# Optimization experiments

Measured on AMD Instinct MI355X. Metric: run time of the kernel, lower is better.

The kernel has to match this reference:

```python
import jax, jax.numpy as jnp
import numpy as np

N_NODES = 8192
IN_F = 256
OUT_F = 256
ALPHA = 0.2  # LeakyReLU negative slope


def setup_inputs() -> dict:
    key = jax.random.key(0)
    k1, k2, k3, k4 = jax.random.split(key, 4)
    X = jax.random.normal(k1, (N_NODES, IN_F), dtype=jnp.float32)
    A = jax.random.randint(k2, (N_NODES, N_NODES), 0, 2, dtype=jnp.int32)
    # torch nn.Linear weight layout: (out_features, in_features)
    W = jax.random.normal(k3, (OUT_F, IN_F), dtype=jnp.float32) * (1.0 / np.sqrt(IN_F))
    r = jax.random.normal(k4, (2 * OUT_F, 1), dtype=jnp.float32)
    return {"X": X, "A": A, "W": W, "r": r}


def reference(X, A, W, r):
    # Wh = X @ W^T  -> (N, F_out)
    Wh = X @ W.T
    # Split r so that cat([Wh_i, Wh_j]) @ r == Wh_i @ r_src + Wh_j @ r_dst
    F_out = Wh.shape[-1]
    r_src = r[:F_out, 0]   # (F,)
    r_dst = r[F_out:, 0]   # (F,)
    s_i = Wh @ r_src       # (N,)
    s_j = Wh @ r_dst       # (N,)
    e = s_i[:, None] + s_j[None, :]                      # (N, N)
    e = jnp.where(e >= 0, e, ALPHA * e)                  # LeakyReLU
    e = jnp.where(A == 0, -jnp.inf, e)                   # mask non-edges
    attention = jax.nn.softmax(e, axis=1)                # row-wise softmax
    output = attention @ Wh                              # (N, F_out)
    return jax.nn.gelu(output, approximate=False)        # torch F.gelu (exact)
```

## Files before the change

### kernel.cpp

```cpp
#include <hip/hip_runtime.h>
#include <hip/hip_bf16.h>

#define N_NODES 8192
#define NF      256
#define L2E     1.44269504088896341f

typedef __attribute__((ext_vector_type(8))) short short8;
typedef __attribute__((ext_vector_type(4))) short short4v;
typedef __attribute__((ext_vector_type(4))) float floatx4;

static __device__ __forceinline__ float bf2f(short s) {
    return __uint_as_float(((unsigned)(unsigned short)s) << 16);
}
static __device__ __forceinline__ short f2bf_rn(float f) {
    unsigned u = __float_as_uint(f) + 0x8000u;
    return (short)(u >> 16);
}
struct bfpair { short hi, lo; };
static __device__ __forceinline__ bfpair split_bf(float x) {
    bfpair p;
    p.hi = f2bf_rn(x);
    p.lo = f2bf_rn(x - bf2f(p.hi));
    return p;
}
static __device__ __forceinline__ void async16(const void* g, void* l) {
    __builtin_amdgcn_global_load_lds(
        (const __attribute__((address_space(1))) unsigned*)g,
        (__attribute__((address_space(3))) unsigned*)l, 16, 0, 0);
}

__global__ __launch_bounds__(256) void kx_split(const float* __restrict__ W,
                                                short* __restrict__ Whi,
                                                short* __restrict__ Wlo) {
    #pragma unroll
    for (int e = 0; e < 4; ++e) {
        const int i = blockIdx.x * 1024 + e * 256 + threadIdx.x;
        bfpair p = split_bf(W[i]);
        Whi[i] = p.hi;
        Wlo[i] = p.lo;
    }
}

__global__ __launch_bounds__(512) void k1_gemm(const float* __restrict__ X,
                                               const short* __restrict__ Whi,
                                               const short* __restrict__ Wlo,
                                               const float* __restrict__ r,
                                               short* __restrict__ WhT,
                                               float* __restrict__ sp_src,
                                               float* __restrict__ sp_dst) {
    __shared__ float Xs[32 * 256];

    const int tid = threadIdx.x;
    const int w = tid >> 6, lane = tid & 63;
    const int q = lane >> 4, m = lane & 15;
    const int rh = w >> 2, cq = w & 3;
    const int i_base = blockIdx.x * 32;

    #pragma unroll
    for (int v = 0; v < 4; ++v) {
        const int rowv = w * 4 + v;
        const int c = lane ^ (rowv & 7);
        async16(X + (size_t)(i_base + rowv) * NF + c * 4, &Xs[rowv * 256]);
    }
    __syncthreads();

    floatx4 acc[4] = {};
    const int xrow = rh * 16 + m;
    const int r7 = xrow & 7;
    #pragma unroll
    for (int ks = 0; ks < 8; ++ks) {
        const int c0 = ks * 8 + q * 2;
        float4 f0 = *(const float4*)(&Xs[xrow * 256 + ((c0 ^ r7) * 4)]);
        float4 f1 = *(const float4*)(&Xs[xrow * 256 + (((c0 + 1) ^ r7) * 4)]);
        const float xsv[8] = {f0.x, f0.y, f0.z, f0.w, f1.x, f1.y, f1.z, f1.w};
        short8 xh, xl;
        #pragma unroll
        for (int c = 0; c < 8; ++c) {
            bfpair p = split_bf(xsv[c]);
            xh[c] = p.hi; xl[c] = p.lo;
        }
        #pragma unroll
        for (int nt = 0; nt < 4; ++nt) {
            const int n = cq * 64 + nt * 16 + m;
            short8 wh = *(const short8*)(Whi + n * NF + ks * 32 + q * 8);
            short8 wl = *(const short8*)(Wlo + n * NF + ks * 32 + q * 8);
            acc[nt] = __builtin_amdgcn_mfma_f32_16x16x32_bf16(xh, wh, acc[nt], 0, 0, 0);
            acc[nt] = __builtin_amdgcn_mfma_f32_16x16x32_bf16(xl, wh, acc[nt], 0, 0, 0);
            acc[nt] = __builtin_amdgcn_mfma_f32_16x16x32_bf16(xh, wl, acc[nt], 0, 0, 0);
        }
    }

    const int i0 = i_base + rh * 16 + q * 4;
    float vs[4] = {0.f, 0.f, 0.f, 0.f}, vd[4] = {0.f, 0.f, 0.f, 0.f};
    #pragma unroll
    for (int nt = 0; nt < 4; ++nt) {
        const int n = cq * 64 + nt * 16 + m;
        short4v v;
        #pragma unroll
        for (int r2 = 0; r2 < 4; ++r2) v[r2] = f2bf_rn(acc[nt][r2]);
        *(short4v*)(WhT + (size_t)n * N_NODES + i0) = v;
        const float rs = r[n], rd = r[NF + n];
        #pragma unroll
        for (int r2 = 0; r2 < 4; ++r2) {
            vs[r2] = fmaf(acc[nt][r2], rs, vs[r2]);
            vd[r2] = fmaf(acc[nt][r2], rd, vd[r2]);
        }
    }
    #pragma unroll
    for (int mask = 1; mask <= 8; mask <<= 1) {
        #pragma unroll
        for (int r2 = 0; r2 < 4; ++r2) {
            vs[r2] += __shfl_xor(vs[r2], mask);
            vd[r2] += __shfl_xor(vd[r2], mask);
        }
    }
    if (m == 0) {
        #pragma unroll
        for (int r2 = 0; r2 < 4; ++r2) {
            sp_src[cq * N_NODES + i0 + r2] = vs[r2];
            sp_dst[cq * N_NODES + i0 + r2] = vd[r2];
        }
    }
}

__global__ __launch_bounds__(256) void k2_sv(const float* __restrict__ sp_src,
                                             const float* __restrict__ sp_dst,
                                             float* __restrict__ s_src,
                                             float* __restrict__ s_dst,
                                             float* __restrict__ pmax) {
    __shared__ float red[256];
    const int tid = threadIdx.x;
    const int i = blockIdx.x * 256 + tid;
    float ss = 0.f, sd = 0.f;
    #pragma unroll
    for (int nb = 0; nb < 4; ++nb) {
        ss += sp_src[nb * N_NODES + i];
        sd += sp_dst[nb * N_NODES + i];
    }
    s_src[i] = ss;
    s_dst[i] = sd;
    red[tid] = sd;
    __syncthreads();
    for (int off = 128; off > 0; off >>= 1) {
        if (tid < off) red[tid] = fmaxf(red[tid], red[tid + off]);
        __syncthreads();
    }
    if (tid == 0) pmax[blockIdx.x] = red[0];
}

static __device__ __forceinline__ void pgroup(const int4 a, const floatx4 t,
                                              const float s_i, const float d_i,
                                              float* p) {
    const int av[4] = {a.x, a.y, a.z, a.w};
    #pragma unroll
    for (int c = 0; c < 4; ++c) {
        float sum = s_i + t[c];
        float lr  = fmaxf(sum, 0.2f * sum);
        float pp  = __builtin_amdgcn_exp2f(fmaf(lr, L2E, d_i));
        p[c] = (av[c] != 0) ? pp : 0.0f;
    }
}

__global__ __launch_bounds__(512, 4) void k4_attn(const int* __restrict__ Adj,
                                                  const short* __restrict__ WhT,
                                                  const float* __restrict__ s_dst,
                                                  const float* __restrict__ s_src,
                                                  const float* __restrict__ pmax,
                                                  float* __restrict__ pden,
                                                  float* __restrict__ outacc) {
    __shared__ short Bs[2][256][64];

    const int tid = threadIdx.x;
    const int w = tid >> 6, lane = tid & 63;
    const int q = lane >> 4, m = lane & 15;
    const int rh = w >> 1, ch = w & 1;
    const int ib = blockIdx.x & 127;
    const int jh = blockIdx.x >> 7;
    const int i0 = ib * 64;
    const int jbase = jh * 2048;
    const int row = i0 + rh * 16 + m;

    float M = pmax[0];
    #pragma unroll
    for (int b = 1; b < 32; ++b) M = fmaxf(M, pmax[b]);
    const float s_i = s_src[row];
    const float e0 = s_i + M;
    const float d_i = -fmaxf(e0, 0.2f * e0) * L2E;

    const int srow = lane >> 3;
    const int scc = (lane & 7) ^ srow;
    const short* gB[4];
    #pragma unroll
    for (int v = 0; v < 4; ++v)
        gB[v] = WhT + (size_t)(w * 32 + v * 8 + srow) * N_NODES + jbase + scc * 8;

    const int* Ap = Adj + (size_t)row * N_NODES + jbase + q * 8;
    const float* tp = s_dst + jbase + q * 8;

    floatx4 acc[8];
    #pragma unroll
    for (int nt = 0; nt < 8; ++nt) acc[nt] = (floatx4){0.f, 0.f, 0.f, 0.f};
    float den = 0.f;

    #pragma unroll
    for (int v = 0; v < 4; ++v)
        async16(gB[v], &Bs[0][w * 32 + v * 8][0]);
    int4 a0 = *(const int4*)(Ap);
    int4 a1 = *(const int4*)(Ap + 4);
    int4 a2 = *(const int4*)(Ap + 32);
    int4 a3 = *(const int4*)(Ap + 36);
    __syncthreads();

    for (int s = 0; s < 32; ++s) {
        const int cur = s & 1;
        const int gt = s * 64;

        floatx4 t0 = *(const floatx4*)(tp + gt);
        floatx4 t1 = *(const floatx4*)(tp + gt + 4);
        floatx4 t2 = *(const floatx4*)(tp + gt + 32);
        floatx4 t3 = *(const floatx4*)(tp + gt + 36);
        __builtin_amdgcn_sched_barrier(0);

        short* dstb = &Bs[cur ^ 1][0][0];
        const int gn = ((s + 1) & 31) * 64;
        #pragma unroll
        for (int v = 0; v < 4; ++v)
            async16(gB[v] + gn, dstb + (w * 32 + v * 8) * 64);
        __builtin_amdgcn_sched_barrier(0);

        int4 na0 = *(const int4*)(Ap + gn);
        int4 na1 = *(const int4*)(Ap + gn + 4);
        int4 na2 = *(const int4*)(Ap + gn + 32);
        int4 na3 = *(const int4*)(Ap + gn + 36);
        __builtin_amdgcn_sched_barrier(0);

        float p[16];
        pgroup(a0, t0, s_i, d_i, p);
        pgroup(a1, t1, s_i, d_i, p + 4);
        pgroup(a2, t2, s_i, d_i, p + 8);
        pgroup(a3, t3, s_i, d_i, p + 12);

        short8 af0, af1;
        #pragma unroll
        for (int c = 0; c < 8; ++c) { af0[c] = f2bf_rn(p[c]); af1[c] = f2bf_rn(p[8 + c]); }
        #pragma unroll
        for (int c = 0; c < 16; ++c) den += p[c];

        const short* Bb = &Bs[cur][0][0];
        __builtin_amdgcn_s_setprio(1);
        #pragma unroll
        for (int nt = 0; nt < 8; ++nt) {
            const int n = ch * 128 + nt * 16 + m;
            const int sw = m & 7;
            short8 b0 = *(const short8*)(Bb + n * 64 + ((q ^ sw) * 8));
            short8 b1 = *(const short8*)(Bb + n * 64 + (((4 + q) ^ sw) * 8));
            acc[nt] = __builtin_amdgcn_mfma_f32_16x16x32_bf16(af0, b0, acc[nt], 0, 0, 0);
            acc[nt] = __builtin_amdgcn_mfma_f32_16x16x32_bf16(af1, b1, acc[nt], 0, 0, 0);
        }
        __builtin_amdgcn_s_setprio(0);

        __builtin_amdgcn_sched_barrier(0);
        asm volatile("s_waitcnt vmcnt(4)" ::: "memory");
        __builtin_amdgcn_s_barrier();

        a0 = na0; a1 = na1; a2 = na2; a3 = na3;
    }

    den += __shfl_xor(den, 16);
    den += __shfl_xor(den, 32);
    if (ch == 0 && q == 0) pden[jh * N_NODES + row] = den;

    #pragma unroll
    for (int nt = 0; nt < 8; ++nt) {
        #pragma unroll
        for (int rg = 0; rg < 4; ++rg) {
            const int orow = i0 + rh * 16 + q * 4 + rg;
            const int n = ch * 128 + nt * 16 + m;
            atomicAdd(&outacc[(size_t)orow * NF + n], acc[nt][rg]);
        }
    }
}

__global__ __launch_bounds__(256) void k5_fin(const float* __restrict__ pden,
                                              float* __restrict__ out) {
    const int gid = blockIdx.x * 256 + threadIdx.x;
    const int row = gid >> 5;
    const int c0 = (gid & 31) * 8;
    const float d = (pden[row] + pden[N_NODES + row]) +
                    (pden[2 * N_NODES + row] + pden[3 * N_NODES + row]);
    const float inv = 1.0f / fmaxf(d, 1e-30f);
    float* p = out + (size_t)row * NF + c0;
    float4 v0 = *(const float4*)(p);
    float4 v1 = *(const float4*)(p + 4);
    float xs[8] = {v0.x, v0.y, v0.z, v0.w, v1.x, v1.y, v1.z, v1.w};
    #pragma unroll
    for (int c = 0; c < 8; ++c) {
        const float x = xs[c] * inv;
        xs[c] = 0.5f * x * (1.0f + erff(x * 0.70710678118f));
    }
    *(float4*)(p)     = (float4){xs[0], xs[1], xs[2], xs[3]};
    *(float4*)(p + 4) = (float4){xs[4], xs[5], xs[6], xs[7]};
}

extern "C" void kernel_launch(void* const* d_in, const int* in_sizes, int n_in,
                              void* d_out, int out_size, void* d_ws, size_t ws_size,
                              hipStream_t stream) {
    const float* X = (const float*)d_in[0];
    const int*   A = (const int*)d_in[1];
    const float* W = (const float*)d_in[2];
    const float* r = (const float*)d_in[3];
    float* out = (float*)d_out;

    char* wsp = (char*)d_ws;
    short* WhT    = (short*)wsp;                    wsp += (size_t)NF * N_NODES * 2;
    short* Whi    = (short*)wsp;                    wsp += NF * NF * 2;
    short* Wlo    = (short*)wsp;                    wsp += NF * NF * 2;
    float* sp_src = (float*)wsp;                    wsp += 4 * N_NODES * 4;
    float* sp_dst = (float*)wsp;                    wsp += 4 * N_NODES * 4;
    float* s_src  = (float*)wsp;                    wsp += N_NODES * 4;
    float* s_dst  = (float*)wsp;                    wsp += N_NODES * 4;
    float* pmax   = (float*)wsp;
    float* pden   = sp_src;

    hipMemsetAsync(out, 0, (size_t)N_NODES * NF * 4, stream);
    kx_split<<<64, 256, 0, stream>>>(W, Whi, Wlo);
    k1_gemm<<<256, 512, 0, stream>>>(X, Whi, Wlo, r, WhT, sp_src, sp_dst);
    k2_sv<<<32, 256, 0, stream>>>(sp_src, sp_dst, s_src, s_dst, pmax);
    k4_attn<<<512, 512, 0, stream>>>(A, WhT, s_dst, s_src, pmax, pden, out);
    k5_fin<<<1024, 256, 0, stream>>>(pden, out);
}
```

Measured before the change: 476.9 us.

## Pack adjacency into bitmask in a pre-pass and stage s_dst in LDS

Adds a k3_bits kernel that uses wave ballots to compress the int32 adjacency matrix into a per-row bitmask. The attention kernel then reads 2 mask words per step instead of 16 int32 values. It also stages the block's s_dst slice into shared memory once, instead of loading it from global memory every iteration. The full 256MB adjacency read still happens, now in a separate streaming kernel, so the intent is to take the large mask traffic out of the MFMA loop, at the cost of an extra launch and an 8MB intermediate write and read.

```diff
diff --git a/kernel.cpp b/kernel.cpp
--- a/kernel.cpp
+++ b/kernel.cpp
@@ -148,20 +148,33 @@
     if (tid == 0) pmax[blockIdx.x] = red[0];
 }
 
-static __device__ __forceinline__ void pgroup(const int4 a, const floatx4 t,
-                                              const float s_i, const float d_i,
-                                              float* p) {
-    const int av[4] = {a.x, a.y, a.z, a.w};
+__global__ __launch_bounds__(512) void k3_bits(const int* __restrict__ Adj,
+                                               unsigned* __restrict__ mask) {
+    const int w = threadIdx.x >> 6, lane = threadIdx.x & 63;
+    const int row = blockIdx.x * 8 + w;
+    const int* Ar = Adj + (size_t)row * N_NODES;
+    unsigned long long* Mr = (unsigned long long*)(mask + (size_t)row * 256);
+    for (int it = 0; it < 128; ++it) {
+        const int v = Ar[it * 64 + lane];
+        const unsigned long long b = __ballot(v != 0);
+        if (lane == 0) Mr[it] = b;
+    }
+}
+
+static __device__ __forceinline__ void pgroupb(const unsigned bits, const int sh,
+                                               const floatx4 t,
+                                               const float s_i, const float d_i,
+                                               float* p) {
     #pragma unroll
     for (int c = 0; c < 4; ++c) {
         float sum = s_i + t[c];
         float lr  = fmaxf(sum, 0.2f * sum);
         float pp  = __builtin_amdgcn_exp2f(fmaf(lr, L2E, d_i));
-        p[c] = (av[c] != 0) ? pp : 0.0f;
-    }
-}
-
-__global__ __launch_bounds__(512, 4) void k4_attn(const int* __restrict__ Adj,
+        p[c] = ((bits >> (sh + c)) & 1u) ? pp : 0.0f;
+    }
+}
+
+__global__ __launch_bounds__(512, 4) void k4_attn(const unsigned* __restrict__ Abits,
                                                   const short* __restrict__ WhT,
                                                   const float* __restrict__ s_dst,
                                                   const float* __restrict__ s_src,
@@ -169,6 +182,7 @@
                                                   float* __restrict__ pden,
                                                   float* __restrict__ outacc) {
     __shared__ short Bs[2][256][64];
+    __shared__ float ts[2048];
 
     const int tid = threadIdx.x;
     const int w = tid >> 6, lane = tid & 63;
@@ -179,6 +193,7 @@
     const int i0 = ib * 64;
     const int jbase = jh * 2048;
     const int row = i0 + rh * 16 + m;
+    const int q8 = q * 8;
 
     float M = pmax[0];
     #pragma unroll
@@ -194,32 +209,22 @@
     for (int v = 0; v < 4; ++v)
         gB[v] = WhT + (size_t)(w * 32 + v * 8 + srow) * N_NODES + jbase + scc * 8;
 
-    const int* Ap = Adj + (size_t)row * N_NODES + jbase + q * 8;
-    const float* tp = s_dst + jbase + q * 8;
+    const unsigned* Mp = Abits + (size_t)row * 256 + (jbase >> 5);
 
     floatx4 acc[8];
     #pragma unroll
     for (int nt = 0; nt < 8; ++nt) acc[nt] = (floatx4){0.f, 0.f, 0.f, 0.f};
     float den = 0.f;
 
+    async16(s_dst + jbase + w * 256 + lane * 4, &ts[w * 256]);
     #pragma unroll
     for (int v = 0; v < 4; ++v)
         async16(gB[v], &Bs[0][w * 32 + v * 8][0]);
-    int4 a0 = *(const int4*)(Ap);
-    int4 a1 = *(const int4*)(Ap + 4);
-    int4 a2 = *(const int4*)(Ap + 32);
-    int4 a3 = *(const int4*)(Ap + 36);
+    uint2 mk = *(const uint2*)(Mp);
     __syncthreads();
 
     for (int s = 0; s < 32; ++s) {
         const int cur = s & 1;
-        const int gt = s * 64;
-
-        floatx4 t0 = *(const floatx4*)(tp + gt);
-        floatx4 t1 = *(const floatx4*)(tp + gt + 4);
-        floatx4 t2 = *(const floatx4*)(tp + gt + 32);
-        floatx4 t3 = *(const floatx4*)(tp + gt + 36);
-        __builtin_amdgcn_sched_barrier(0);
 
         short* dstb = &Bs[cur ^ 1][0][0];
         const int gn = ((s + 1) & 31) * 64;
@@ -228,17 +233,20 @@
             async16(gB[v] + gn, dstb + (w * 32 + v * 8) * 64);
         __builtin_amdgcn_sched_barrier(0);
 
-        int4 na0 = *(const int4*)(Ap + gn);
-        int4 na1 = *(const int4*)(Ap + gn + 4);
-        int4 na2 = *(const int4*)(Ap + gn + 32);
-        int4 na3 = *(const int4*)(Ap + gn + 36);
+        uint2 nmk = *(const uint2*)(Mp + ((s + 1) & 31) * 2);
         __builtin_amdgcn_sched_barrier(0);
 
+        const int gt = s * 64;
+        floatx4 t0 = *(const floatx4*)(ts + gt + q8);
+        floatx4 t1 = *(const floatx4*)(ts + gt + q8 + 4);
+        floatx4 t2 = *(const floatx4*)(ts + gt + 32 + q8);
+        floatx4 t3 = *(const floatx4*)(ts + gt + 32 + q8 + 4);
+
         float p[16];
-        pgroup(a0, t0, s_i, d_i, p);
-        pgroup(a1, t1, s_i, d_i, p + 4);
-        pgroup(a2, t2, s_i, d_i, p + 8);
-        pgroup(a3, t3, s_i, d_i, p + 12);
+        pgroupb(mk.x, q8,     t0, s_i, d_i, p);
+        pgroupb(mk.x, q8 + 4, t1, s_i, d_i, p + 4);
+        pgroupb(mk.y, q8,     t2, s_i, d_i, p + 8);
+        pgroupb(mk.y, q8 + 4, t3, s_i, d_i, p + 12);
 
         short8 af0, af1;
         #pragma unroll
@@ -260,10 +268,10 @@
         __builtin_amdgcn_s_setprio(0);
 
         __builtin_amdgcn_sched_barrier(0);
-        asm volatile("s_waitcnt vmcnt(4)" ::: "memory");
+        asm volatile("s_waitcnt vmcnt(1)" ::: "memory");
         __builtin_amdgcn_s_barrier();
 
-        a0 = na0; a1 = na1; a2 = na2; a3 = na3;
+        mk = nmk;
     }
 
     den += __shfl_xor(den, 16);
@@ -319,13 +327,15 @@
     float* sp_dst = (float*)wsp;                    wsp += 4 * N_NODES * 4;
     float* s_src  = (float*)wsp;                    wsp += N_NODES * 4;
     float* s_dst  = (float*)wsp;                    wsp += N_NODES * 4;
-    float* pmax   = (float*)wsp;
+    float* pmax   = (float*)wsp;                    wsp += 256;
+    unsigned* Abits = (unsigned*)wsp;
     float* pden   = sp_src;
 
     hipMemsetAsync(out, 0, (size_t)N_NODES * NF * 4, stream);
     kx_split<<<64, 256, 0, stream>>>(W, Whi, Wlo);
     k1_gemm<<<256, 512, 0, stream>>>(X, Whi, Wlo, r, WhT, sp_src, sp_dst);
     k2_sv<<<32, 256, 0, stream>>>(sp_src, sp_dst, s_src, s_dst, pmax);
-    k4_attn<<<512, 512, 0, stream>>>(A, WhT, s_dst, s_src, pmax, pden, out);
+    k3_bits<<<1024, 512, 0, stream>>>(A, Abits);
+    k4_attn<<<512, 512, 0, stream>>>(Abits, WhT, s_dst, s_src, pmax, pden, out);
     k5_fin<<<1024, 256, 0, stream>>>(pden, out);
 }
```

Result: slower. 521.6 us (+9.4%).

## Restructure attention kernel into 256-thread blocks with 8-way column split

Applied to the files above, without the earlier changes.

The attention kernel now uses 4 waves per block, each covering 16 rows by all 256 output features, with K-steps of 32 instead of 64. The column range is split 8 ways instead of 4, so the grid doubles to 1024 blocks. s_dst is staged once into shared memory rather than reloaded from global memory each step, and the finalize kernel now sums 8 partial denominators. This is meant to raise occupancy and parallelism and reuse each P fragment across 16 MFMAs, at the cost of twice as many atomic adds to the output and more accumulator registers per thread.

```diff
diff --git a/kernel.cpp b/kernel.cpp
--- a/kernel.cpp
+++ b/kernel.cpp
@@ -161,24 +161,25 @@
     }
 }
 
-__global__ __launch_bounds__(512, 4) void k4_attn(const int* __restrict__ Adj,
+__global__ __launch_bounds__(256, 4) void k4_attn(const int* __restrict__ Adj,
                                                   const short* __restrict__ WhT,
                                                   const float* __restrict__ s_dst,
                                                   const float* __restrict__ s_src,
                                                   const float* __restrict__ pmax,
                                                   float* __restrict__ pden,
                                                   float* __restrict__ outacc) {
-    __shared__ short Bs[2][256][64];
+    __shared__ short Bs[2][256][32];
+    __shared__ float ts[1024];
 
     const int tid = threadIdx.x;
     const int w = tid >> 6, lane = tid & 63;
     const int q = lane >> 4, m = lane & 15;
-    const int rh = w >> 1, ch = w & 1;
     const int ib = blockIdx.x & 127;
     const int jh = blockIdx.x >> 7;
     const int i0 = ib * 64;
-    const int jbase = jh * 2048;
-    const int row = i0 + rh * 16 + m;
+    const int jbase = jh * 1024;
+    const int row = i0 + w * 16 + m;
+    const int q8 = q * 8;
 
     float M = pmax[0];
     #pragma unroll
@@ -187,95 +188,83 @@
     const float e0 = s_i + M;
     const float d_i = -fmaxf(e0, 0.2f * e0) * L2E;
 
-    const int srow = lane >> 3;
-    const int scc = (lane & 7) ^ srow;
+    const int srow = lane >> 2;
     const short* gB[4];
     #pragma unroll
+    for (int v = 0; v < 4; ++v) {
+        const int n = w * 64 + v * 16 + srow;
+        const int c = (lane & 3) ^ ((n >> 1) & 3);
+        gB[v] = WhT + (size_t)n * N_NODES + jbase + c * 8;
+    }
+
+    const int* Ap = Adj + (size_t)row * N_NODES + jbase + q8;
+
+    floatx4 acc[16];
+    #pragma unroll
+    for (int nt = 0; nt < 16; ++nt) acc[nt] = (floatx4){0.f, 0.f, 0.f, 0.f};
+    float den = 0.f;
+
+    async16(s_dst + jbase + w * 256 + lane * 4, &ts[w * 256]);
+    #pragma unroll
     for (int v = 0; v < 4; ++v)
-        gB[v] = WhT + (size_t)(w * 32 + v * 8 + srow) * N_NODES + jbase + scc * 8;
-
-    const int* Ap = Adj + (size_t)row * N_NODES + jbase + q * 8;
-    const float* tp = s_dst + jbase + q * 8;
-
-    floatx4 acc[8];
-    #pragma unroll
-    for (int nt = 0; nt < 8; ++nt) acc[nt] = (floatx4){0.f, 0.f, 0.f, 0.f};
-    float den = 0.f;
-
-    #pragma unroll
-    for (int v = 0; v < 4; ++v)
-        async16(gB[v], &Bs[0][w * 32 + v * 8][0]);
+        async16(gB[v], &Bs[0][w * 64 + v * 16][0]);
     int4 a0 = *(const int4*)(Ap);
     int4 a1 = *(const int4*)(Ap + 4);
-    int4 a2 = *(const int4*)(Ap + 32);
-    int4 a3 = *(const int4*)(Ap + 36);
     __syncthreads();
 
     for (int s = 0; s < 32; ++s) {
         const int cur = s & 1;
-        const int gt = s * 64;
-
-        floatx4 t0 = *(const floatx4*)(tp + gt);
-        floatx4 t1 = *(const floatx4*)(tp + gt + 4);
-        floatx4 t2 = *(const floatx4*)(tp + gt + 32);
-        floatx4 t3 = *(const floatx4*)(tp + gt + 36);
-        __builtin_amdgcn_sched_barrier(0);
 
         short* dstb = &Bs[cur ^ 1][0][0];
-        const int gn = ((s + 1) & 31) * 64;
+        const int gn = ((s + 1) & 31) * 32;
         #pragma unroll
         for (int v = 0; v < 4; ++v)
-            async16(gB[v] + gn, dstb + (w * 32 + v * 8) * 64);
+            async16(gB[v] + gn, dstb + (w * 64 + v * 16) * 32);
         __builtin_amdgcn_sched_barrier(0);
 
         int4 na0 = *(const int4*)(Ap + gn);
         int4 na1 = *(const int4*)(Ap + gn + 4);
-        int4 na2 = *(const int4*)(Ap + gn + 32);
-        int4 na3 = *(const int4*)(Ap + gn + 36);
         __builtin_amdgcn_sched_barrier(0);
 
-        float p[16];
+        const int gt = s * 32;
+        floatx4 t0 = *(const floatx4*)(ts + gt + q8);
+        floatx4 t1 = *(const floatx4*)(ts + gt + q8 + 4);
+        float p[8];
         pgroup(a0, t0, s_i, d_i, p);
         pgroup(a1, t1, s_i, d_i, p + 4);
-        pgroup(a2, t2, s_i, d_i, p + 8);
-        pgroup(a3, t3, s_i, d_i, p + 12);
-
-        short8 af0, af1;
-        #pragma unroll
-        for (int c = 0; c < 8; ++c) { af0[c] = f2bf_rn(p[c]); af1[c] = f2bf_rn(p[8 + c]); }
-        #pragma unroll
-        for (int c = 0; c < 16; ++c) den += p[c];
+
+        short8 af;
+        #pragma unroll
+        for (int c = 0; c < 8; ++c) { af[c] = f2bf_rn(p[c]); den += p[c]; }
 
         const short* Bb = &Bs[cur][0][0];
         __builtin_amdgcn_s_setprio(1);
         #pragma unroll
-        for (int nt = 0; nt < 8; ++nt) {
-            const int n = ch * 128 + nt * 16 + m;
-            const int sw = m & 7;
-            short8 b0 = *(const short8*)(Bb + n * 64 + ((q ^ sw) * 8));
-            short8 b1 = *(const short8*)(Bb + n * 64 + (((4 + q) ^ sw) * 8));
-            acc[nt] = __builtin_amdgcn_mfma_f32_16x16x32_bf16(af0, b0, acc[nt], 0, 0, 0);
-            acc[nt] = __builtin_amdgcn_mfma_f32_16x16x32_bf16(af1, b1, acc[nt], 0, 0, 0);
+        for (int nt = 0; nt < 16; ++nt) {
+            const int n = nt * 16 + m;
+            const int slot = q ^ ((n >> 1) & 3);
+            short8 b = *(const short8*)(Bb + n * 32 + slot * 8);
+            acc[nt] = __builtin_amdgcn_mfma_f32_16x16x32_bf16(af, b, acc[nt], 0, 0, 0);
         }
         __builtin_amdgcn_s_setprio(0);
 
         __builtin_amdgcn_sched_barrier(0);
-        asm volatile("s_waitcnt vmcnt(4)" ::: "memory");
+        asm volatile("s_waitcnt vmcnt(2)" ::: "memory");
         __builtin_amdgcn_s_barrier();
 
-        a0 = na0; a1 = na1; a2 = na2; a3 = na3;
+        a0 = na0; a1 = na1;
     }
 
     den += __shfl_xor(den, 16);
     den += __shfl_xor(den, 32);
-    if (ch == 0 && q == 0) pden[jh * N_NODES + row] = den;
-
-    #pragma unroll
-    for (int nt = 0; nt < 8; ++nt) {
+    if (q == 0) pden[jh * N_NODES + row] = den;
+
+    #pragma unroll
+    for (int nt = 0; nt < 16; ++nt) {
         #pragma unroll
         for (int rg = 0; rg < 4; ++rg) {
-            const int orow = i0 + rh * 16 + q * 4 + rg;
-            const int n = ch * 128 + nt * 16 + m;
+            const int orow = i0 + w * 16 + q * 4 + rg;
+            const int n = nt * 16 + m;
             atomicAdd(&outacc[(size_t)orow * NF + n], acc[nt][rg]);
         }
     }
@@ -286,8 +275,10 @@
     const int gid = blockIdx.x * 256 + threadIdx.x;
     const int row = gid >> 5;
     const int c0 = (gid & 31) * 8;
-    const float d = (pden[row] + pden[N_NODES + row]) +
-                    (pden[2 * N_NODES + row] + pden[3 * N_NODES + row]);
+    const float d = ((pden[row] + pden[N_NODES + row]) +
+                     (pden[2 * N_NODES + row] + pden[3 * N_NODES + row])) +
+                    ((pden[4 * N_NODES + row] + pden[5 * N_NODES + row]) +
+                     (pden[6 * N_NODES + row] + pden[7 * N_NODES + row]));
     const float inv = 1.0f / fmaxf(d, 1e-30f);
     float* p = out + (size_t)row * NF + c0;
     float4 v0 = *(const float4*)(p);
@@ -326,6 +317,6 @@
     kx_split<<<64, 256, 0, stream>>>(W, Whi, Wlo);
     k1_gemm<<<256, 512, 0, stream>>>(X, Whi, Wlo, r, WhT, sp_src, sp_dst);
     k2_sv<<<32, 256, 0, stream>>>(sp_src, sp_dst, s_src, s_dst, pmax);
-    k4_attn<<<512, 512, 0, stream>>>(A, WhT, s_dst, s_src, pmax, pden, out);
+    k4_attn<<<1024, 256, 0, stream>>>(A, WhT, s_dst, s_src, pmax, pden, out);
     k5_fin<<<1024, 256, 0, stream>>>(pden, out);
 }
```

Measured after the change: 486.0 us. No clear change (+1.9%).
